# Performance work log

Measured on AMD Instinct MI355X. Metric: run time of the kernel, lower is better.

## Reference

```python
import jax, jax.numpy as jnp
import numpy as np

# Mamba2 config (matches mamba_ssm.Mamba2 defaults used by the wrapper)
D_MODEL = 1024
D_STATE = 128
D_CONV = 4
EXPAND = 2
HEADDIM = 64
CHUNK = 256
D_INNER = EXPAND * D_MODEL            # 2048
NHEADS = D_INNER // HEADDIM           # 32
CONV_DIM = D_INNER + 2 * D_STATE      # 2304 (x, B, C share the causal conv)
D_IN_PROJ = 2 * D_INNER + 2 * D_STATE + NHEADS  # z, xBC, dt
EPS = 1e-5


def rmsnorm(x, w, eps=EPS):
    return x * jax.lax.rsqrt(jnp.mean(x * x, axis=-1, keepdims=True) + eps) * w


def setup_inputs() -> dict:
    key = jax.random.key(0)
    ks = jax.random.split(key, 8)
    B, L = 2, 2048
    def w(k, shape, sc=0.02):
        return jax.random.normal(k, shape, jnp.float32) * sc
    return {
        "x": jax.random.normal(ks[0], (B, L, D_MODEL), jnp.float32),
        "norm_w": jnp.ones((D_MODEL,), jnp.float32),
        "in_proj_w": w(ks[1], (D_IN_PROJ, D_MODEL)),
        "conv_w": w(ks[2], (CONV_DIM, 1, D_CONV), 0.2),   # depthwise kernel
        "conv_b": jnp.zeros((CONV_DIM,), jnp.float32),
        "dt_bias": w(ks[3], (NHEADS,), 1.0),
        "A_log": jnp.log(1.0 + 15.0 * jax.random.uniform(ks[4], (NHEADS,), jnp.float32)),
        "D": jnp.ones((NHEADS,), jnp.float32),
        "gnorm_w": jnp.ones((D_INNER,), jnp.float32),
        "out_proj_w": w(ks[5], (D_MODEL, D_INNER)),
    }


def _ssd(xd, a, Bm, Cm):
    """Chunked SSD scan (ssd_minimal_discrete).
    xd: (b,l,h,p) = x*dt ; a: (b,l,h) = dt*A ; Bm,Cm: (b,l,n) (ngroups=1)."""
    b, l, h, p = xd.shape
    n = Bm.shape[-1]
    nc = l // CHUNK
    xd = xd.reshape(b, nc, CHUNK, h, p)
    a = a.reshape(b, nc, CHUNK, h).transpose(0, 3, 1, 2)   # (b,h,nc,c)
    Bm = Bm.reshape(b, nc, CHUNK, n)
    Cm = Cm.reshape(b, nc, CHUNK, n)
    a_cs = jnp.cumsum(a, axis=-1)                           # (b,h,nc,c)
    # 1) intra-chunk: causal decay matrix L[t,s] = exp(sum_{s<i<=t} a_i)
    diff = a_cs[..., :, None] - a_cs[..., None, :]          # (b,h,nc,c,c)
    mask = jnp.tril(jnp.ones((CHUNK, CHUNK), bool))
    Lm = jnp.exp(jnp.where(mask, diff, 0.0)) * mask
    Y_diag = jnp.einsum("bcln,bcsn,bhcls,bcshp->bclhp", Cm, Bm, Lm, xd)
    # 2) per-chunk end states
    decay_states = jnp.exp(a_cs[..., -1:] - a_cs)           # (b,h,nc,c)
    states = jnp.einsum("bcln,bhcl,bclhp->bchpn", Bm, decay_states, xd)
    # 3) inter-chunk recurrence (vectorized segsum over the 8+1 chunk totals)
    tot = jnp.pad(a_cs[..., -1], ((0, 0), (0, 0), (1, 0)))  # (b,h,nc+1)
    tot_cs = jnp.cumsum(tot, axis=-1)
    dchunk = tot_cs[..., :, None] - tot_cs[..., None, :]    # (b,h,nc+1,nc+1)
    cmask = jnp.tril(jnp.ones((nc + 1, nc + 1), bool))
    dchunk = jnp.exp(jnp.where(cmask, dchunk, 0.0)) * cmask
    states = jnp.concatenate([jnp.zeros_like(states[:, :1]), states], axis=1)
    new_states = jnp.einsum("bhzc,bchpn->bzhpn", dchunk, states)
    init_states = new_states[:, :-1]                        # state entering each chunk
    # 4) state -> output contribution
    Y_off = jnp.einsum("bcln,bchpn,bhcl->bclhp", Cm, init_states, jnp.exp(a_cs))
    return (Y_diag + Y_off).reshape(b, l, h, p)


def reference(x, norm_w, in_proj_w, conv_w, conv_b, dt_bias, A_log, D, gnorm_w, out_proj_w):
    res = x
    u = rmsnorm(x, norm_w)
    zxbcdt = u @ in_proj_w.T                                # (b,l,d_in_proj)
    z, xBC, dt = jnp.split(zxbcdt, [D_INNER, D_INNER + CONV_DIM], axis=-1)
    # causal depthwise conv1d over (x,B,C), then SiLU
    xBC_t = jnp.pad(xBC.transpose(0, 2, 1), ((0, 0), (0, 0), (D_CONV - 1, 0)))
    conv = jax.lax.conv_general_dilated(
        xBC_t, conv_w, (1,), "VALID",
        dimension_numbers=("NCH", "OIH", "NCH"), feature_group_count=CONV_DIM)
    xBC = jax.nn.silu(conv.transpose(0, 2, 1) + conv_b)
    xs, Bm, Cm = jnp.split(xBC, [D_INNER, D_INNER + D_STATE], axis=-1)
    dt = jax.nn.softplus(dt + dt_bias)                      # (b,l,h)
    A = -jnp.exp(A_log)                                     # (h,)
    xh = xs.reshape(xs.shape[0], xs.shape[1], NHEADS, HEADDIM)
    y = _ssd(xh * dt[..., None], dt * A, Bm, Cm)
    y = y + D[None, None, :, None] * xh                     # skip term
    y = y.reshape(xs.shape)
    y = rmsnorm(y * jax.nn.silu(z), gnorm_w)                # gated RMSNorm
    return res + y @ out_proj_w.T
```

## Files before the change

### kernel.cpp

```cpp
#include <hip/hip_runtime.h>
#include <hip/hip_bf16.h>

typedef __hip_bfloat16 bf16_t;
typedef __attribute__((ext_vector_type(8))) short bfrag8;
typedef __attribute__((ext_vector_type(4))) float floatx4;

#define DM     1024
#define DI     2048
#define NHD    32
#define HD     64
#define DSTATE 128
#define CONVD  2304
#define NPROJ  4384
#define NPAD   4480
#define MR     4096
#define LL     2048
#define EPSF   1e-5f
#define LOG2E  1.44269504088896f

__device__ __forceinline__ void gl_lds16(const void* g, void* l) {
  __builtin_amdgcn_global_load_lds((const __attribute__((address_space(1))) void*)g,
                                   (__attribute__((address_space(3))) void*)l, 16, 0, 0);
}
__device__ __forceinline__ unsigned pack_bf16_rn(float a, float b) {
  unsigned ua = (__float_as_uint(a) + 0x8000u) >> 16;
  unsigned ub = (__float_as_uint(b) + 0x8000u) >> 16;
  return ua | (ub << 16);
}
__device__ __forceinline__ unsigned short bf16u(float a) {
  return (unsigned short)((__float_as_uint(a) + 0x8000u) >> 16);
}
__device__ __forceinline__ float blo(unsigned u){ return __uint_as_float(u << 16); }
__device__ __forceinline__ float bhi(unsigned u){ return __uint_as_float(u & 0xffff0000u); }
__device__ __forceinline__ void unp8(uint4 u, float* v) {
  v[0]=blo(u.x); v[1]=bhi(u.x); v[2]=blo(u.y); v[3]=bhi(u.y);
  v[4]=blo(u.z); v[5]=bhi(u.z); v[6]=blo(u.w); v[7]=bhi(u.w);
}
typedef union { unsigned u[4]; bfrag8 f; } fragu;

#define W1CNT (NPAD * DM / 4)
#define W2CNT (DM * DI / 4)
#define CVTBLK ((W1CNT + W2CNT) / 256)
__global__ void rms_cvt_kernel(const float* __restrict__ x, const float* __restrict__ w,
                               bf16_t* __restrict__ ub,
                               const float* __restrict__ w1, const float* __restrict__ w2,
                               const float* __restrict__ gw,
                               bf16_t* __restrict__ o1, bf16_t* __restrict__ o2) {
  __shared__ float red[4];
  int t = threadIdx.x;
  if (blockIdx.x < MR) {
    int row = blockIdx.x;
    float4 v = ((const float4*)(x + (long)row * DM))[t];
    float ss = v.x*v.x + v.y*v.y + v.z*v.z + v.w*v.w;
#pragma unroll
    for (int off = 32; off > 0; off >>= 1) ss += __shfl_down(ss, off, 64);
    if ((t & 63) == 0) red[t >> 6] = ss;
    __syncthreads();
    float tot = red[0] + red[1] + red[2] + red[3];
    float rs = rsqrtf(tot * (1.f / DM) + EPSF);
    float4 wv = ((const float4*)w)[t];
    bf16_t* o = ub + (long)row * DM + t * 4;
    o[0] = __float2bfloat16(v.x * rs * wv.x);
    o[1] = __float2bfloat16(v.y * rs * wv.y);
    o[2] = __float2bfloat16(v.z * rs * wv.z);
    o[3] = __float2bfloat16(v.w * rs * wv.w);
  } else {
    int i4 = (blockIdx.x - MR) * 256 + t;
    if (i4 < W1CNT) {
      int idx = i4 * 4;
      int row = idx >> 10;
      float4 v = make_float4(0.f, 0.f, 0.f, 0.f);
      if (row < NPROJ) v = *(const float4*)(w1 + idx);
      bf16_t* d = o1 + idx;
      d[0] = __float2bfloat16(v.x); d[1] = __float2bfloat16(v.y);
      d[2] = __float2bfloat16(v.z); d[3] = __float2bfloat16(v.w);
    } else {
      int idx = (i4 - W1CNT) * 4;
      int k = idx & (DI - 1);
      float4 v = *(const float4*)(w2 + idx);
      float4 g = *(const float4*)(gw + k);
      bf16_t* d = o2 + idx;
      d[0] = __float2bfloat16(v.x * g.x); d[1] = __float2bfloat16(v.y * g.y);
      d[2] = __float2bfloat16(v.z * g.z); d[3] = __float2bfloat16(v.w * g.w);
    }
  }
}

template<int TN, bool DO_RES, bool OUT_BF16>
__global__ __launch_bounds__(256) void gemm64_kernel(const bf16_t* __restrict__ A,
    const bf16_t* __restrict__ Bw, const float* __restrict__ resid,
    const float* __restrict__ ssqp, void* __restrict__ Cout, int N, int K) {
  __shared__ bf16_t As[128 * 64];
  __shared__ bf16_t Bs[TN * 64];
  __shared__ float rsS[128];
  const int tid = threadIdx.x;
  const int lane = tid & 63;
  const int wv = tid >> 6;
  const int l15 = lane & 15;
  const int l4 = lane >> 4;
  constexpr int MF = (TN == 128) ? 4 : 2;
  const int wm = (TN == 128) ? ((wv >> 1) << 6) : (wv << 5);
  const int wn = (TN == 128) ? ((wv & 1) << 6) : 0;
  int tm, tn;
  if (DO_RES) {
    const int flat = blockIdx.y * gridDim.x + blockIdx.x;
    const int xcd = flat & 7, ridx = flat >> 3;
    tm = ((xcd & 3) * 8 + (ridx & 7)) << 7;
    tn = ((xcd >> 2) * 8 + (ridx >> 3)) * TN;
  } else {
    tm = blockIdx.x << 7;
    tn = blockIdx.y * TN;
  }

  if (DO_RES) {
    int rr = tid >> 1;
    const float4* pp = (const float4*)(ssqp + (long)(tm + rr) * 32 + (tid & 1) * 16);
    float s = 0.f;
#pragma unroll
    for (int q = 0; q < 4; q++) { float4 v = pp[q]; s += v.x + v.y + v.z + v.w; }
    s += __shfl_xor(s, 1, 64);
    if ((tid & 1) == 0) rsS[rr] = rsqrtf(s * (1.f / DI) + EPSF);
  }

  floatx4 acc[MF][4];
#pragma unroll
  for (int i = 0; i < MF; i++)
#pragma unroll
    for (int j = 0; j < 4; j++) acc[i][j] = (floatx4){0.f, 0.f, 0.f, 0.f};

  const int r = tid >> 3;
  const int c8 = tid & 7;
  const int scol = ((c8 ^ (r & 7)) << 3);
  const bf16_t* Ag = A + (long)(tm + r) * K + scol;
  const bf16_t* Bg = Bw + (long)(tn + r) * K + scol;
  const int swz = l15 & 7;

  for (int k0 = 0; k0 < K; k0 += 64) {
#pragma unroll
    for (int q = 0; q < 4; q++)
      gl_lds16(Ag + (long)(q * 32) * K + k0, &As[q * 2048 + tid * 8]);
#pragma unroll
    for (int q = 0; q < TN / 32; q++)
      gl_lds16(Bg + (long)(q * 32) * K + k0, &Bs[q * 2048 + tid * 8]);
    __syncthreads();
#pragma unroll
    for (int kk = 0; kk < 2; kk++) {
      bfrag8 af[MF], bfr[4];
      const int ch = ((kk << 2) | l4) ^ swz;
#pragma unroll
      for (int j = 0; j < 4; j++)
        bfr[j] = *(const bfrag8*)&Bs[(wn + j * 16 + l15) * 64 + ch * 8];
#pragma unroll
      for (int i = 0; i < MF; i++)
        af[i] = *(const bfrag8*)&As[(wm + i * 16 + l15) * 64 + ch * 8];
#pragma unroll
      for (int i = 0; i < MF; i++)
#pragma unroll
        for (int j = 0; j < 4; j++)
          acc[i][j] = __builtin_amdgcn_mfma_f32_16x16x32_bf16(af[i], bfr[j], acc[i][j], 0, 0, 0);
    }
    __syncthreads();
  }
#pragma unroll
  for (int i = 0; i < MF; i++)
#pragma unroll
    for (int j = 0; j < 4; j++)
#pragma unroll
      for (int r2 = 0; r2 < 4; r2++) {
        int row = tm + wm + i * 16 + l4 * 4 + r2;
        int col = tn + wn + j * 16 + l15;
        float v = acc[i][j][r2];
        if (OUT_BF16) {
          ((bf16_t*)Cout)[(long)row * N + col] = __float2bfloat16(v);
        } else {
          if (DO_RES) v = v * rsS[row - tm] + resid[(long)row * N + col];
          ((float*)Cout)[(long)row * N + col] = v;
        }
      }
}

__global__ __launch_bounds__(512, 2) void gemm256_kernel(const bf16_t* __restrict__ A,
    const bf16_t* __restrict__ Bw, bf16_t* __restrict__ Cout) {
  __shared__ bf16_t lds[65536];
  const int t = threadIdx.x;

  if (blockIdx.x >= 256) {
    const int idx = blockIdx.x - 256;
    const int mi = idx & 31, ni = idx >> 5;
    const int hh = t >> 8;
    const int tl = t & 255;
    const int lane = tl & 63, wv = tl >> 6;
    const int l15 = lane & 15, l4 = lane >> 4;
    const int wm = wv << 5;
    const int tm = mi * 128;
    const int tn = 4096 + ni * 64;
    bf16_t* As = lds + hh * 12288;
    bf16_t* Bs = As + 8192;
    float* Rf = (float*)((char*)lds + 49152);
    floatx4 acc[2][4];
#pragma unroll
    for (int i = 0; i < 2; i++)
#pragma unroll
      for (int j = 0; j < 4; j++) acc[i][j] = (floatx4){0.f, 0.f, 0.f, 0.f};
    const int r = tl >> 3;
    const int c8 = tl & 7;
    const int scol = ((c8 ^ (r & 7)) << 3);
    const int kbase = hh * 512;
    const bf16_t* Ag = A + (long)(tm + r) * DM + kbase + scol;
    const bf16_t* Bg = Bw + (long)(tn + r) * DM + kbase + scol;
    const int swz = l15 & 7;
    for (int k0 = 0; k0 < 512; k0 += 64) {
#pragma unroll
      for (int q = 0; q < 4; q++)
        gl_lds16(Ag + (long)(q * 32) * DM + k0, &As[q * 2048 + tl * 8]);
#pragma unroll
      for (int q = 0; q < 2; q++)
        gl_lds16(Bg + (long)(q * 32) * DM + k0, &Bs[q * 2048 + tl * 8]);
      __syncthreads();
#pragma unroll
      for (int kk = 0; kk < 2; kk++) {
        bfrag8 af[2], bfr[4];
        const int ch = ((kk << 2) | l4) ^ swz;
#pragma unroll
        for (int j = 0; j < 4; j++)
          bfr[j] = *(const bfrag8*)&Bs[(j * 16 + l15) * 64 + ch * 8];
#pragma unroll
        for (int i = 0; i < 2; i++)
          af[i] = *(const bfrag8*)&As[(wm + i * 16 + l15) * 64 + ch * 8];
#pragma unroll
        for (int i = 0; i < 2; i++)
#pragma unroll
          for (int j = 0; j < 4; j++)
            acc[i][j] = __builtin_amdgcn_mfma_f32_16x16x32_bf16(af[i], bfr[j], acc[i][j], 0, 0, 0);
      }
      __syncthreads();
    }
    if (hh == 1) {
#pragma unroll
      for (int i = 0; i < 2; i++)
#pragma unroll
        for (int j = 0; j < 4; j++)
#pragma unroll
          for (int r2 = 0; r2 < 4; r2++)
            Rf[(wm + i * 16 + l4 * 4 + r2) * 65 + j * 16 + l15] = acc[i][j][r2];
    }
    __syncthreads();
    if (hh == 0) {
#pragma unroll
      for (int i = 0; i < 2; i++)
#pragma unroll
        for (int j = 0; j < 4; j++)
#pragma unroll
          for (int r2 = 0; r2 < 4; r2++) {
            int rr = wm + i * 16 + l4 * 4 + r2;
            int cc = j * 16 + l15;
            float v = acc[i][j][r2] + Rf[rr * 65 + cc];
            Cout[(long)(tm + rr) * NPAD + tn + cc] = __float2bfloat16(v);
          }
    }
    return;
  }

  const int lane = t & 63, wv = t >> 6;
  const int wm = wv >> 2, wn = wv & 3;
  const int l15 = lane & 15, l4 = lane >> 4;
  const int xcd = blockIdx.x & 7, idx = blockIdx.x >> 3;
  const int bx = (xcd & 3) * 4 + (idx & 3);
  const int by = (xcd >> 2) * 8 + (idx >> 2);
  const int tm = bx << 8, tn = by << 8;

  const int srow = t >> 3;
  const int scol = ((t & 7) ^ (srow & 7)) << 3;
  const bf16_t* Ag = A + (long)(tm + srow) * DM + scol;
  const bf16_t* Bg = Bw + (long)(tn + srow) * DM + scol;
  bf16_t* Asl = lds;
  bf16_t* Bsl = lds + 32768;
  const int swl = (l15 & 7) << 4;
  const int ca0 = (l4 * 16) ^ swl;
  const int ca1 = (64 + l4 * 16) ^ swl;

  floatx4 acc[8][4];
#pragma unroll
  for (int i = 0; i < 8; i++)
#pragma unroll
    for (int j = 0; j < 4; j++) acc[i][j] = (floatx4){0.f, 0.f, 0.f, 0.f};
  bfrag8 bq[8];

#define STG_A(tt, h) { \
  bf16_t* d_ = Asl + (((tt) & 1) * 2 + (h)) * 8192 + t * 8; \
  gl_lds16(Ag + (long)((h) * 128     ) * DM + (tt) * 64, d_); \
  gl_lds16(Ag + (long)((h) * 128 + 64) * DM + (tt) * 64, d_ + 4096); \
}
#define STG_B(tt, h) { \
  bf16_t* d_ = Bsl + (((tt) & 1) * 2 + (h)) * 8192 + t * 8; \
  gl_lds16(Bg + (long)((h) * 128     ) * DM + (tt) * 64, d_); \
  gl_lds16(Bg + (long)((h) * 128 + 64) * DM + (tt) * 64, d_ + 4096); \
}
#define PH(d, q, STG, WT) { \
  const char* Ah_ = (const char*)(Asl + ((d) * 2 + wm) * 8192); \
  const char* Bh_ = (const char*)(Bsl + ((d) * 2 + (wn >> 1)) * 8192); \
  if ((q) == 0) { \
    _Pragma("unroll") \
    for (int j = 0; j < 4; j++) { \
      int r_ = ((wn & 1) << 6) + j * 16 + l15; \
      bq[j * 2]     = *(const bfrag8*)(Bh_ + r_ * 128 + ca0); \
      bq[j * 2 + 1] = *(const bfrag8*)(Bh_ + r_ * 128 + ca1); \
    } \
  } \
  bfrag8 aq0, aq1, aq2, aq3; \
  { int r_ = (q) * 32 + l15; \
    aq0 = *(const bfrag8*)(Ah_ + r_ * 128 + ca0); \
    aq1 = *(const bfrag8*)(Ah_ + r_ * 128 + ca1); \
    aq2 = *(const bfrag8*)(Ah_ + (r_ + 16) * 128 + ca0); \
    aq3 = *(const bfrag8*)(Ah_ + (r_ + 16) * 128 + ca1); } \
  STG; \
  __builtin_amdgcn_s_barrier(); \
  asm volatile("s_waitcnt lgkmcnt(0)" ::: "memory"); \
  __builtin_amdgcn_s_setprio(1); \
  _Pragma("unroll") \
  for (int j = 0; j < 4; j++) { \
    acc[(q)*2  ][j] = __builtin_amdgcn_mfma_f32_16x16x32_bf16(aq0, bq[j*2],   acc[(q)*2  ][j], 0, 0, 0); \
    acc[(q)*2  ][j] = __builtin_amdgcn_mfma_f32_16x16x32_bf16(aq1, bq[j*2+1], acc[(q)*2  ][j], 0, 0, 0); \
    acc[(q)*2+1][j] = __builtin_amdgcn_mfma_f32_16x16x32_bf16(aq2, bq[j*2],   acc[(q)*2+1][j], 0, 0, 0); \
    acc[(q)*2+1][j] = __builtin_amdgcn_mfma_f32_16x16x32_bf16(aq3, bq[j*2+1], acc[(q)*2+1][j], 0, 0, 0); \
  } \
  __builtin_amdgcn_s_setprio(0); \
  WT; \
  __builtin_amdgcn_s_barrier(); \
}

  STG_A(0, 0); STG_A(0, 1); STG_B(0, 0); STG_B(0, 1);
  STG_B(1, 0); STG_B(1, 1);
  asm volatile("s_waitcnt vmcnt(4)" ::: "memory");
  __builtin_amdgcn_s_barrier();

  for (int it = 0; it < 7; ++it) {
    const int ta = 2 * it, tb = ta + 1;
    PH(0, 0, STG_A(tb, 0), {})
    PH(0, 1, STG_A(tb, 1), {})
    PH(0, 2, STG_B(ta + 2, 0), {})
    PH(0, 3, STG_B(ta + 2, 1), asm volatile("s_waitcnt vmcnt(4)" ::: "memory");)
    PH(1, 0, STG_A(ta + 2, 0), {})
    PH(1, 1, STG_A(ta + 2, 1), {})
    PH(1, 2, STG_B(tb + 2, 0), {})
    PH(1, 3, STG_B(tb + 2, 1), asm volatile("s_waitcnt vmcnt(4)" ::: "memory");)
  }
  {
    PH(0, 0, STG_A(15, 0), {})
    PH(0, 1, STG_A(15, 1), {})
    PH(0, 2, {}, {})
    PH(0, 3, {}, asm volatile("s_waitcnt vmcnt(0)" ::: "memory");)
    PH(1, 0, {}, {})
    PH(1, 1, {}, {})
    PH(1, 2, {}, {})
    PH(1, 3, {}, {})
  }
#undef PH
#undef STG_A
#undef STG_B

  const long crow = tm + wm * 128;
  const int ccol = tn + wn * 64;
#pragma unroll
  for (int qi = 0; qi < 8; qi++)
#pragma unroll
    for (int j = 0; j < 4; j++)
#pragma unroll
      for (int r2 = 0; r2 < 4; r2++) {
        long row = crow + (qi >> 1) * 32 + (qi & 1) * 16 + l4 * 4 + r2;
        int col = ccol + j * 16 + l15;
        Cout[row * NPAD + col] = __float2bfloat16(acc[qi][j][r2]);
      }
}

__global__ __launch_bounds__(256) void sst_kernel(const bf16_t* __restrict__ xdT,
    const bf16_t* __restrict__ BmT, bf16_t* __restrict__ states,
    const bf16_t* __restrict__ Cmh, const bf16_t* __restrict__ Bmh,
    bf16_t* __restrict__ SL, const float* __restrict__ acs,
    const float* __restrict__ ctot) {
  __shared__ bf16_t As[128 * 32];
  __shared__ bf16_t Bs[128 * 32];
  const int t = threadIdx.x, lane = t & 63, wv = t >> 6;
  const int l15 = lane & 15, l4 = lane >> 4;
  if (blockIdx.x < 512) {
    int blk = blockIdx.x;
    int bc = blk >> 5;
    floatx4 acc[2][4];
#pragma unroll
    for (int i = 0; i < 2; i++)
#pragma unroll
      for (int j = 0; j < 4; j++) acc[i][j] = (floatx4){0.f, 0.f, 0.f, 0.f};
    const bf16_t* arow = BmT + (long)bc * 128 * 256;
    const bf16_t* brow = xdT + (long)blk * 64 * 256;
    const float* acsb = acs + (long)blk * 256;
    const float at = ctot[blk];
#pragma unroll
    for (int kt = 0; kt < 8; kt++) {
      const int lbase = kt * 32 + l4 * 8;
      float e[8];
      *(float4*)&e[0] = *(const float4*)(acsb + lbase);
      *(float4*)&e[4] = *(const float4*)(acsb + lbase + 4);
#pragma unroll
      for (int q = 0; q < 8; q++) e[q] = exp2f(at - e[q]);
      bfrag8 af[2];
      fragu bfr[4];
#pragma unroll
      for (int i = 0; i < 2; i++)
        af[i] = *(const bfrag8*)(arow + (long)(wv * 32 + i * 16 + l15) * 256 + lbase);
#pragma unroll
      for (int j = 0; j < 4; j++) {
        uint4 u = *(const uint4*)(brow + (long)(j * 16 + l15) * 256 + lbase);
        float v[8];
        unp8(u, v);
#pragma unroll
        for (int q2 = 0; q2 < 4; q2++)
          bfr[j].u[q2] = pack_bf16_rn(v[q2 * 2] * e[q2 * 2], v[q2 * 2 + 1] * e[q2 * 2 + 1]);
      }
#pragma unroll
      for (int i = 0; i < 2; i++)
#pragma unroll
        for (int j = 0; j < 4; j++)
          acc[i][j] = __builtin_amdgcn_mfma_f32_16x16x32_bf16(af[i], bfr[j].f, acc[i][j], 0, 0, 0);
    }
#pragma unroll
    for (int i = 0; i < 2; i++)
#pragma unroll
      for (int j = 0; j < 4; j++) {
        int n_base = wv * 32 + i * 16 + l4 * 4;
        int p = j * 16 + l15;
        unsigned lo = pack_bf16_rn(acc[i][j][0], acc[i][j][1]);
        unsigned hi = pack_bf16_rn(acc[i][j][2], acc[i][j][3]);
        *(uint2*)(states + (long)blk * 8192 + p * 128 + n_base) = make_uint2(lo, hi);
      }
  } else {
    int idx = blockIdx.x - 512;
    const int bc = idx >> 2;
    const int tm = ((idx >> 1) & 1) << 7;
    const int tn = (idx & 1) << 7;
    const int wm = (wv >> 1) << 6;
    const int wn = (wv & 1) << 6;
    floatx4 acc[4][4];
#pragma unroll
    for (int i = 0; i < 4; i++)
#pragma unroll
      for (int j = 0; j < 4; j++) acc[i][j] = (floatx4){0.f, 0.f, 0.f, 0.f};
    const int arow = t >> 2;
    const int acol = (t & 3) << 3;
    const bf16_t* Ag = Cmh + (long)bc * 256 * DSTATE + (long)(tm + arow) * DSTATE + acol;
    const bf16_t* Bg = Bmh + (long)bc * 256 * DSTATE + (long)(tn + arow) * DSTATE + acol;
    const long k64 = (long)64 * DSTATE;
    for (int k0 = 0; k0 < DSTATE; k0 += 32) {
      gl_lds16(Ag + k0, &As[t * 8]);
      gl_lds16(Ag + k64 + k0, &As[2048 + t * 8]);
      gl_lds16(Bg + k0, &Bs[t * 8]);
      gl_lds16(Bg + k64 + k0, &Bs[2048 + t * 8]);
      __syncthreads();
      bfrag8 af[4], bfr[4];
#pragma unroll
      for (int i = 0; i < 4; i++)
        af[i] = *(const bfrag8*)&As[(wm + i * 16 + l15) * 32 + l4 * 8];
#pragma unroll
      for (int j = 0; j < 4; j++)
        bfr[j] = *(const bfrag8*)&Bs[(wn + j * 16 + l15) * 32 + l4 * 8];
#pragma unroll
      for (int i = 0; i < 4; i++)
#pragma unroll
        for (int j = 0; j < 4; j++)
          acc[i][j] = __builtin_amdgcn_mfma_f32_16x16x32_bf16(af[i], bfr[j], acc[i][j], 0, 0, 0);
      __syncthreads();
    }
    bf16_t* Cb = SL + (long)bc * 65536;
#pragma unroll
    for (int i = 0; i < 4; i++)
#pragma unroll
      for (int j = 0; j < 4; j++)
#pragma unroll
        for (int r = 0; r < 4; r++)
          Cb[(long)(tm + wm + i * 16 + l4 * 4 + r) * 256 + tn + wn + j * 16 + l15] =
              __float2bfloat16(acc[i][j][r]);
  }
}

__global__ __launch_bounds__(256) void conv4_kernel(const bf16_t* __restrict__ zxh,
    const float* __restrict__ cw, const float* __restrict__ cb,
    bf16_t* __restrict__ xhb, bf16_t* __restrict__ Bmh, bf16_t* __restrict__ Cmh) {
  int g = blockIdx.x * 256 + threadIdx.x;
  int cg = g % 288;
  int blt = g / 288;
  int c0 = cg * 8;
  long bl0 = (long)blt * 4;
  int l0 = (int)(bl0 & (LL - 1));
  const bf16_t* base = zxh + bl0 * NPAD + DI + c0;
  float rv[7][8];
#pragma unroll
  for (int j = 0; j < 7; j++) {
    int dj = j - 3;
    if (l0 + dj >= 0) {
      uint4 u = *(const uint4*)(base + (long)dj * NPAD);
      unp8(u, rv[j]);
    } else {
#pragma unroll
      for (int q = 0; q < 8; q++) rv[j][q] = 0.f;
    }
  }
  float4 wq[8];
#pragma unroll
  for (int q = 0; q < 8; q++) wq[q] = ((const float4*)cw)[c0 + q];
  float bias[8];
  *(float4*)&bias[0] = *(const float4*)(cb + c0);
  *(float4*)&bias[4] = *(const float4*)(cb + c0 + 4);
#pragma unroll
  for (int i = 0; i < 4; i++) {
    unsigned o[4];
#pragma unroll
    for (int q2 = 0; q2 < 4; q2++) {
      float rr[2];
#pragma unroll
      for (int e = 0; e < 2; e++) {
        int q = q2 * 2 + e;
        float a = bias[q] + wq[q].x * rv[i][q] + wq[q].y * rv[i + 1][q]
                + wq[q].z * rv[i + 2][q] + wq[q].w * rv[i + 3][q];
        rr[e] = a / (1.f + __expf(-a));
      }
      o[q2] = pack_bf16_rn(rr[0], rr[1]);
    }
    uint4 ov = make_uint4(o[0], o[1], o[2], o[3]);
    long bl = bl0 + i;
    if (c0 < DI)               *(uint4*)(xhb + bl * DI + c0) = ov;
    else if (c0 < DI + DSTATE) *(uint4*)(Bmh + bl * DSTATE + (c0 - DI)) = ov;
    else                       *(uint4*)(Cmh + bl * DSTATE + (c0 - DI - DSTATE)) = ov;
  }
}

__global__ __launch_bounds__(256) void xdt_kernel(const bf16_t* __restrict__ xhb,
    const bf16_t* __restrict__ Bmh, const bf16_t* __restrict__ zxh,
    const float* __restrict__ A_log, const float* __restrict__ dtb,
    float* __restrict__ acs, float* __restrict__ ctot,
    bf16_t* __restrict__ xdT, bf16_t* __restrict__ BmT) {
  __shared__ unsigned short Tb[9216];
  __shared__ float acsL[256];
  __shared__ float dtsL[256];
  __shared__ float wsum[4];
  int blk = blockIdx.x;
  int t = threadIdx.x;
  if (blk < 512) {
    int h = blk & 31, bc = blk >> 5;
    {
      int lane = t & 63, w = t >> 6;
      float Ah = -__expf(A_log[h]) * LOG2E;
      int gl = bc * 256 + t;
      float vv = __bfloat162float(zxh[(long)gl * NPAD + (NPROJ - 32) + h]) + dtb[h];
      float sp = fmaxf(vv, 0.f) + log1pf(__expf(-fabsf(vv)));
      float a = sp * Ah;
#pragma unroll
      for (int off = 1; off < 64; off <<= 1) {
        float v = __shfl_up(a, off, 64);
        if (lane >= off) a += v;
      }
      if (lane == 63) wsum[w] = a;
      __syncthreads();
      float base = 0.f;
      for (int i = 0; i < 4; i++) base += (i < w) ? wsum[i] : 0.f;
      a += base;
      acsL[t] = a;
      dtsL[t] = sp;
      acs[blk * 256 + t] = a;
      if (t == 255) ctot[blk] = a;
      __syncthreads();
    }
    unsigned short* T1 = Tb;
    int l_loc = t >> 2, pg = t & 3;
    for (int lt = 0; lt < 4; lt++) {
      int ll = lt * 64 + l_loc;
      int gl = bc * 256 + ll;
      float w1 = dtsL[ll];
      const uint4* src = (const uint4*)(xhb + (long)gl * DI + h * HD + pg * 16);
      uint4 u0 = src[0], u1 = src[1];
      float v[16];
      unp8(u0, v); unp8(u1, v + 8);
      __syncthreads();
#pragma unroll
      for (int q = 0; q < 16; q++)
        T1[(pg * 16 + q) * 72 + l_loc] = bf16u(v[q] * w1);
      __syncthreads();
      long orow = ((long)blk * 64 + l_loc) * 256 + lt * 64 + pg * 16;
      *(uint4*)(xdT + orow)     = *(uint4*)&T1[l_loc * 72 + pg * 16];
      *(uint4*)(xdT + orow + 8) = *(uint4*)&T1[l_loc * 72 + pg * 16 + 8];
    }
  } else {
    unsigned short* T = Tb;
    int bc = blk - 512;
    int l_loc = t >> 2, ng = t & 3;
    for (int lt = 0; lt < 4; lt++) {
      int gl = bc * 256 + lt * 64 + l_loc;
      const uint4* src = (const uint4*)(Bmh + (long)gl * DSTATE + ng * 32);
      uint4 u[4];
#pragma unroll
      for (int q = 0; q < 4; q++) u[q] = src[q];
      __syncthreads();
      const unsigned short* us = (const unsigned short*)u;
#pragma unroll
      for (int e = 0; e < 32; e++)
        T[(ng * 32 + e) * 72 + l_loc] = us[e];
      __syncthreads();
      int n = t >> 1, lg2 = t & 1;
      long orow = ((long)bc * 128 + n) * 256 + lt * 64 + lg2 * 32;
#pragma unroll
      for (int q = 0; q < 4; q++)
        *(uint4*)(BmT + orow + q * 8) = *(uint4*)&T[n * 72 + lg2 * 32 + q * 8];
    }
  }
}

__global__ void scan_kernel(const bf16_t* __restrict__ states, const float* __restrict__ ctot,
                            bf16_t* __restrict__ initsb) {
  int id = blockIdx.x * 256 + threadIdx.x;
  int pn = id & 8191;
  int bh = id >> 13;
  int b = bh >> 5, h = bh & 31;
  float S = 0.f;
#pragma unroll
  for (int c = 0; c < 8; c++) {
    int blk = (b * 8 + c) * 32 + h;
    initsb[(long)blk * 8192 + pn] = __float2bfloat16(S);
    S = exp2f(ctot[blk]) * S + __bfloat162float(states[(long)blk * 8192 + pn]);
  }
}

__global__ __launch_bounds__(512, 4) void yk4_kernel(const bf16_t* __restrict__ SL,
     const bf16_t* __restrict__ Cmh, const bf16_t* __restrict__ xhb,
     const bf16_t* __restrict__ zxh, const float* __restrict__ acs,
     const bf16_t* __restrict__ initsb, const bf16_t* __restrict__ xdT,
     const float* __restrict__ Dp, bf16_t* __restrict__ yg, float* __restrict__ ssqp) {
  int bi = blockIdx.x;
  int bc = (bi & 7) * 2 + ((bi >> 3) & 1);
  int h = bi >> 4;
  int ablk = bc * 32 + h;
  int t = threadIdx.x;
  int wv = t >> 6;
  int mh = wv >> 2, wsub = wv & 3;
  int lane = t & 63;
  int l15 = lane & 15, l4 = lane >> 4;

  __shared__ float acsS[256];
  __shared__ __align__(16) char bbuf[49152];
  bf16_t* xds = (bf16_t*)bbuf;
  bf16_t* ins = (bf16_t*)(bbuf + 32768);
  float* Yt = (float*)bbuf;

  {
    const bf16_t* xrow_g = xdT + (long)ablk * 64 * 256;
#pragma unroll
    for (int it = 0; it < 4; it++) {
      int sl = it * 512 + t;
      int p = sl >> 5, s = sl & 31;
      int c = (s & 24) | ((s & 7) ^ (p & 7));
      gl_lds16(xrow_g + p * 256 + c * 8, &xds[sl * 8]);
    }
    const bf16_t* irow_g = initsb + (long)ablk * 8192;
#pragma unroll
    for (int it = 0; it < 2; it++) {
      int sl = it * 512 + t;
      int p = sl >> 4, s = sl & 15;
      int c = (s & 8) | ((s & 7) ^ (p & 7));
      gl_lds16(irow_g + p * 128 + c * 8, &ins[sl * 8]);
    }
  }
  if (t < 256) acsS[t] = acs[ablk * 256 + t];
  __syncthreads();

  const int rowbase = bc * 256;
  const int l0 = mh * 128 + wsub * 32 + l15;
  const int l1 = l0 + 16;
  const float al0 = acsS[l0], al1 = acsS[l1];
  const float eA0 = exp2f(al0), eA1 = exp2f(al1);
  const bf16_t* SL0 = SL + (long)bc * 65536 + (long)l0 * 256;
  const bf16_t* SL1 = SL + (long)bc * 65536 + (long)l1 * 256;

  floatx4 acc[2][4];
#pragma unroll
  for (int i = 0; i < 2; i++)
#pragma unroll
    for (int j = 0; j < 4; j++) acc[i][j] = (floatx4){0.f, 0.f, 0.f, 0.f};

  const int nkd = (mh + 1) * 4;
  for (int kt = 0; kt < nkd; kt++) {
    int sbase = kt * 32 + l4 * 8;
    float as[8];
    *(float4*)&as[0] = *(const float4*)&acsS[sbase];
    *(float4*)&as[4] = *(const float4*)&acsS[sbase + 4];
    float sv0[8], sv1[8];
    unp8(*(const uint4*)(SL0 + sbase), sv0);
    unp8(*(const uint4*)(SL1 + sbase), sv1);
    fragu af0, af1;
#pragma unroll
    for (int q2 = 0; q2 < 4; q2++) {
      float p00, p01, p10, p11;
      {
        int s = sbase + q2 * 2;
        float d0 = al0 - as[q2 * 2], d1 = al0 - as[q2 * 2 + 1];
        p00 = (s <= l0) ? sv0[q2 * 2] * exp2f(fminf(d0, 0.f)) : 0.f;
        p01 = (s + 1 <= l0) ? sv0[q2 * 2 + 1] * exp2f(fminf(d1, 0.f)) : 0.f;
        float e0 = al1 - as[q2 * 2], e1 = al1 - as[q2 * 2 + 1];
        p10 = (s <= l1) ? sv1[q2 * 2] * exp2f(fminf(e0, 0.f)) : 0.f;
        p11 = (s + 1 <= l1) ? sv1[q2 * 2 + 1] * exp2f(fminf(e1, 0.f)) : 0.f;
      }
      af0.u[q2] = pack_bf16_rn(p00, p01);
      af1.u[q2] = pack_bf16_rn(p10, p11);
    }
    bfrag8 bfr[4];
    int ch = kt * 4 + l4;
#pragma unroll
    for (int j = 0; j < 4; j++) {
      int p = j * 16 + l15;
      int sw = (ch & 24) | ((ch & 7) ^ (p & 7));
      bfr[j] = *(const bfrag8*)&xds[(p * 32 + sw) * 8];
    }
#pragma unroll
    for (int j = 0; j < 4; j++) {
      acc[0][j] = __builtin_amdgcn_mfma_f32_16x16x32_bf16(af0.f, bfr[j], acc[0][j], 0, 0, 0);
      acc[1][j] = __builtin_amdgcn_mfma_f32_16x16x32_bf16(af1.f, bfr[j], acc[1][j], 0, 0, 0);
    }
  }
#pragma unroll
  for (int kt = 0; kt < 4; kt++) {
    int n0 = kt * 32 + l4 * 8;
    uint4 c0 = *(const uint4*)(Cmh + (long)(rowbase + l0) * DSTATE + n0);
    uint4 c1 = *(const uint4*)(Cmh + (long)(rowbase + l1) * DSTATE + n0);
    float cv0[8], cv1[8];
    unp8(c0, cv0); unp8(c1, cv1);
    fragu af0, af1;
#pragma unroll
    for (int q2 = 0; q2 < 4; q2++) {
      af0.u[q2] = pack_bf16_rn(cv0[q2 * 2] * eA0, cv0[q2 * 2 + 1] * eA0);
      af1.u[q2] = pack_bf16_rn(cv1[q2 * 2] * eA1, cv1[q2 * 2 + 1] * eA1);
    }
    bfrag8 bfr[4];
    int ch = kt * 4 + l4;
#pragma unroll
    for (int j = 0; j < 4; j++) {
      int p = j * 16 + l15;
      int sw = (ch & 8) | ((ch & 7) ^ (p & 7));
      bfr[j] = *(const bfrag8*)&ins[(p * 16 + sw) * 8];
    }
#pragma unroll
    for (int j = 0; j < 4; j++) {
      acc[0][j] = __builtin_amdgcn_mfma_f32_16x16x32_bf16(af0.f, bfr[j], acc[0][j], 0, 0, 0);
      acc[1][j] = __builtin_amdgcn_mfma_f32_16x16x32_bf16(af1.f, bfr[j], acc[1][j], 0, 0, 0);
    }
  }
  float Dh = Dp[h];
#pragma unroll
  for (int pass = 0; pass < 2; pass++) {
    __syncthreads();
    if (mh == pass) {
#pragma unroll
      for (int i = 0; i < 2; i++)
#pragma unroll
        for (int j = 0; j < 4; j++)
#pragma unroll
          for (int r = 0; r < 4; r++)
            Yt[(wsub * 32 + i * 16 + l4 * 4 + r) * 66 + j * 16 + l15] = acc[i][j][r];
    }
    __syncthreads();
    {
      int row_l = t >> 2;
      int chc = (t & 3) * 16;
      long rowg = rowbase + pass * 128 + row_l;
      float ss = 0.f;
#pragma unroll
      for (int it = 0; it < 2; it++) {
        int c = chc + it * 8;
        float4 y0 = *(const float4*)&Yt[row_l * 66 + c];
        float4 y1 = *(const float4*)&Yt[row_l * 66 + c + 4];
        uint4 ux = *(const uint4*)(xhb + rowg * DI + h * HD + c);
        uint4 uz = *(const uint4*)(zxh + rowg * NPAD + h * HD + c);
        float xv[8], zv[8];
        unp8(ux, xv); unp8(uz, zv);
        float yv[8] = {y0.x, y0.y, y0.z, y0.w, y1.x, y1.y, y1.z, y1.w};
        unsigned o[4];
#pragma unroll
        for (int q = 0; q < 4; q++) {
          float v0 = (yv[q * 2 + 0] + Dh * xv[q * 2 + 0]) *
                     (zv[q * 2 + 0] / (1.f + __expf(-zv[q * 2 + 0])));
          float v1 = (yv[q * 2 + 1] + Dh * xv[q * 2 + 1]) *
                     (zv[q * 2 + 1] / (1.f + __expf(-zv[q * 2 + 1])));
          ss += v0 * v0 + v1 * v1;
          o[q] = pack_bf16_rn(v0, v1);
        }
        *(uint4*)(yg + rowg * DI + h * HD + c) = make_uint4(o[0], o[1], o[2], o[3]);
      }
      ss += __shfl_xor(ss, 1, 64);
      ss += __shfl_xor(ss, 2, 64);
      if ((t & 3) == 0) ssqp[rowg * 32 + h] = ss;
    }
  }
}

extern "C" void kernel_launch(void* const* d_in, const int* in_sizes, int n_in,
                              void* d_out, int out_size, void* d_ws, size_t ws_size,
                              hipStream_t stream) {
  const float* x    = (const float*)d_in[0];
  const float* nw   = (const float*)d_in[1];
  const float* w1   = (const float*)d_in[2];
  const float* cw   = (const float*)d_in[3];
  const float* cb   = (const float*)d_in[4];
  const float* dtb  = (const float*)d_in[5];
  const float* alog = (const float*)d_in[6];
  const float* Dp   = (const float*)d_in[7];
  const float* gw   = (const float*)d_in[8];
  const float* w2   = (const float*)d_in[9];
  float* out = (float*)d_out;

  char* ws = (char*)d_ws;
  size_t off = 0;
  auto alloc = [&](size_t bytes) -> void* {
    void* p = ws + off;
    off += (bytes + 255) & ~(size_t)255;
    return p;
  };
  bf16_t* ub     = (bf16_t*)alloc((size_t)MR * DM * 2);
  bf16_t* w1b    = (bf16_t*)alloc((size_t)NPAD * DM * 2);
  bf16_t* w2b    = (bf16_t*)alloc((size_t)DM * DI * 2);
  bf16_t* zxh    = (bf16_t*)alloc((size_t)MR * NPAD * 2);
  bf16_t* xhb    = (bf16_t*)alloc((size_t)MR * DI * 2);
  bf16_t* Bmh    = (bf16_t*)alloc((size_t)MR * DSTATE * 2);
  bf16_t* Cmh    = (bf16_t*)alloc((size_t)MR * DSTATE * 2);
  bf16_t* SL     = (bf16_t*)alloc((size_t)16 * 256 * 256 * 2);
  float* acs     = (float*)alloc((size_t)512 * 256 * 4);
  float* ctot    = (float*)alloc((size_t)512 * 4);
  bf16_t* states = (bf16_t*)alloc((size_t)512 * 8192 * 2);
  bf16_t* initsb = (bf16_t*)alloc((size_t)512 * 8192 * 2);
  bf16_t* xdT    = (bf16_t*)alloc((size_t)512 * 64 * 256 * 2);
  bf16_t* BmT    = (bf16_t*)alloc((size_t)16 * 128 * 256 * 2);
  bf16_t* yg     = (bf16_t*)alloc((size_t)MR * DI * 2);
  float* ssqp    = (float*)alloc((size_t)MR * NHD * 4);
  if (off > ws_size) return;

  rms_cvt_kernel<<<MR + CVTBLK, 256, 0, stream>>>(x, nw, ub, w1, w2, gw, w1b, w2b);
  gemm256_kernel<<<416, 512, 0, stream>>>(ub, w1b, zxh);
  conv4_kernel<<<(1024 * 288) / 256, 256, 0, stream>>>(zxh, cw, cb, xhb, Bmh, Cmh);
  xdt_kernel<<<528, 256, 0, stream>>>(xhb, Bmh, zxh, alog, dtb, acs, ctot, xdT, BmT);
  sst_kernel<<<576, 256, 0, stream>>>(xdT, BmT, states, Cmh, Bmh, SL, acs, ctot);
  scan_kernel<<<(2 * 32 * 8192) / 256, 256, 0, stream>>>(states, ctot, initsb);
  yk4_kernel<<<512, 512, 0, stream>>>(SL, Cmh, xhb, zxh, acs, initsb, xdT, Dp, yg, ssqp);
  gemm64_kernel<64, true, false><<<dim3(MR / 128, DM / 64), 256, 0, stream>>>(
      yg, w2b, x, ssqp, out, DM, DI);
}
```

Measured before the change: 246.8 us.

## Share B-tile across two M halves in 512-thread out-projection GEMM

Result: no change. 250.1 us (+1.4%).

```diff
diff --git a/kernel.cpp b/kernel.cpp
--- a/kernel.cpp
+++ b/kernel.cpp
@@ -86,75 +86,72 @@
   }
 }
 
-template<int TN, bool DO_RES, bool OUT_BF16>
-__global__ __launch_bounds__(256) void gemm64_kernel(const bf16_t* __restrict__ A,
+__global__ __launch_bounds__(512) void outproj_kernel(const bf16_t* __restrict__ A,
     const bf16_t* __restrict__ Bw, const float* __restrict__ resid,
-    const float* __restrict__ ssqp, void* __restrict__ Cout, int N, int K) {
-  __shared__ bf16_t As[128 * 64];
-  __shared__ bf16_t Bs[TN * 64];
-  __shared__ float rsS[128];
-  const int tid = threadIdx.x;
-  const int lane = tid & 63;
-  const int wv = tid >> 6;
-  const int l15 = lane & 15;
-  const int l4 = lane >> 4;
-  constexpr int MF = (TN == 128) ? 4 : 2;
-  const int wm = (TN == 128) ? ((wv >> 1) << 6) : (wv << 5);
-  const int wn = (TN == 128) ? ((wv & 1) << 6) : 0;
-  int tm, tn;
-  if (DO_RES) {
-    const int flat = blockIdx.y * gridDim.x + blockIdx.x;
-    const int xcd = flat & 7, ridx = flat >> 3;
-    tm = ((xcd & 3) * 8 + (ridx & 7)) << 7;
-    tn = ((xcd >> 2) * 8 + (ridx >> 3)) * TN;
-  } else {
-    tm = blockIdx.x << 7;
-    tn = blockIdx.y * TN;
-  }
-
-  if (DO_RES) {
-    int rr = tid >> 1;
-    const float4* pp = (const float4*)(ssqp + (long)(tm + rr) * 32 + (tid & 1) * 16);
+    const float* __restrict__ ssqp, float* __restrict__ Cout) {
+  __shared__ bf16_t As2[2][128 * 64];
+  __shared__ bf16_t Bs[64 * 64];
+  __shared__ float rsS[256];
+  const int t = threadIdx.x;
+  const int hh = t >> 8;
+  const int tl = t & 255;
+  const int lane = tl & 63, wv = tl >> 6;
+  const int l15 = lane & 15, l4 = lane >> 4;
+  const int wm = wv << 5;
+  const int b = blockIdx.x;
+  const int xcd = b & 7, idx = b >> 3;
+  const int bx = (xcd & 3) * 4 + (idx & 3);
+  const int by = (xcd >> 2) * 8 + (idx >> 2);
+  const int tmb = bx << 8;
+  const int tm = tmb + hh * 128;
+  const int tn = by << 6;
+
+  {
+    int rr = t >> 1;
+    const float4* pp = (const float4*)(ssqp + (long)(tmb + rr) * 32 + (t & 1) * 16);
     float s = 0.f;
 #pragma unroll
     for (int q = 0; q < 4; q++) { float4 v = pp[q]; s += v.x + v.y + v.z + v.w; }
     s += __shfl_xor(s, 1, 64);
-    if ((tid & 1) == 0) rsS[rr] = rsqrtf(s * (1.f / DI) + EPSF);
-  }
-
-  floatx4 acc[MF][4];
-#pragma unroll
-  for (int i = 0; i < MF; i++)
+    if ((t & 1) == 0) rsS[rr] = rsqrtf(s * (1.f / DI) + EPSF);
+  }
+
+  floatx4 acc[2][4];
+#pragma unroll
+  for (int i = 0; i < 2; i++)
 #pragma unroll
     for (int j = 0; j < 4; j++) acc[i][j] = (floatx4){0.f, 0.f, 0.f, 0.f};
 
-  const int r = tid >> 3;
-  const int c8 = tid & 7;
+  const int r = tl >> 3;
+  const int c8 = tl & 7;
   const int scol = ((c8 ^ (r & 7)) << 3);
-  const bf16_t* Ag = A + (long)(tm + r) * K + scol;
-  const bf16_t* Bg = Bw + (long)(tn + r) * K + scol;
+  const bf16_t* Ag = A + (long)(tm + r) * DI + scol;
+  const bf16_t* Bg = Bw + (long)(tn + r) * DI + scol;
   const int swz = l15 & 7;
-
-  for (int k0 = 0; k0 < K; k0 += 64) {
+  bf16_t* As = &As2[hh][0];
+
+  for (int k0 = 0; k0 < DI; k0 += 64) {
 #pragma unroll
     for (int q = 0; q < 4; q++)
-      gl_lds16(Ag + (long)(q * 32) * K + k0, &As[q * 2048 + tid * 8]);
-#pragma unroll
-    for (int q = 0; q < TN / 32; q++)
-      gl_lds16(Bg + (long)(q * 32) * K + k0, &Bs[q * 2048 + tid * 8]);
+      gl_lds16(Ag + (long)(q * 32) * DI + k0, &As[q * 2048 + tl * 8]);
+    if (hh == 0) {
+#pragma unroll
+      for (int q = 0; q < 2; q++)
+        gl_lds16(Bg + (long)(q * 32) * DI + k0, &Bs[q * 2048 + tl * 8]);
+    }
     __syncthreads();
 #pragma unroll
     for (int kk = 0; kk < 2; kk++) {
-      bfrag8 af[MF], bfr[4];
+      bfrag8 af[2], bfr[4];
       const int ch = ((kk << 2) | l4) ^ swz;
 #pragma unroll
       for (int j = 0; j < 4; j++)
-        bfr[j] = *(const bfrag8*)&Bs[(wn + j * 16 + l15) * 64 + ch * 8];
-#pragma unroll
-      for (int i = 0; i < MF; i++)
+        bfr[j] = *(const bfrag8*)&Bs[(j * 16 + l15) * 64 + ch * 8];
+#pragma unroll
+      for (int i = 0; i < 2; i++)
         af[i] = *(const bfrag8*)&As[(wm + i * 16 + l15) * 64 + ch * 8];
 #pragma unroll
-      for (int i = 0; i < MF; i++)
+      for (int i = 0; i < 2; i++)
 #pragma unroll
         for (int j = 0; j < 4; j++)
           acc[i][j] = __builtin_amdgcn_mfma_f32_16x16x32_bf16(af[i], bfr[j], acc[i][j], 0, 0, 0);
@@ -162,20 +159,15 @@
     __syncthreads();
   }
 #pragma unroll
-  for (int i = 0; i < MF; i++)
+  for (int i = 0; i < 2; i++)
 #pragma unroll
     for (int j = 0; j < 4; j++)
 #pragma unroll
       for (int r2 = 0; r2 < 4; r2++) {
         int row = tm + wm + i * 16 + l4 * 4 + r2;
-        int col = tn + wn + j * 16 + l15;
-        float v = acc[i][j][r2];
-        if (OUT_BF16) {
-          ((bf16_t*)Cout)[(long)row * N + col] = __float2bfloat16(v);
-        } else {
-          if (DO_RES) v = v * rsS[row - tm] + resid[(long)row * N + col];
-          ((float*)Cout)[(long)row * N + col] = v;
-        }
+        int col = tn + j * 16 + l15;
+        float v = acc[i][j][r2] * rsS[row - tmb] + resid[(long)row * DM + col];
+        Cout[(long)row * DM + col] = v;
       }
 }
 
@@ -844,6 +836,5 @@
   sst_kernel<<<576, 256, 0, stream>>>(xdT, BmT, states, Cmh, Bmh, SL, acs, ctot);
   scan_kernel<<<(2 * 32 * 8192) / 256, 256, 0, stream>>>(states, ctot, initsb);
   yk4_kernel<<<512, 512, 0, stream>>>(SL, Cmh, xhb, zxh, acs, initsb, xdT, Dp, yg, ssqp);
-  gemm64_kernel<64, true, false><<<dim3(MR / 128, DM / 64), 256, 0, stream>>>(
-      yg, w2b, x, ssqp, out, DM, DI);
-}
+  outproj_kernel<<<256, 512, 0, stream>>>(yg, w2b, x, ssqp, out);
+}
```
